# Optimization experiments

Measured on AMD Instinct MI355X. Metric: run time of the kernel, lower is better.

The kernel has to match this reference:

```python
import jax, jax.numpy as jnp
import numpy as np

MAX_TOKENS = 8192
MAX_NUM_NODES = 8192
FEATURES = 256


def setup_inputs() -> dict:
    key = jax.random.key(0)
    k_emb, k_start, k_end = jax.random.split(key, 3)
    embedding = jax.random.normal(k_emb, (MAX_NUM_NODES, FEATURES), dtype=jnp.float32)
    node_span_starts = jax.random.randint(k_start, (MAX_NUM_NODES,), 0, 4096, dtype=jnp.int32)
    node_span_ends = jax.random.randint(k_end, (MAX_NUM_NODES,), 0, MAX_TOKENS, dtype=jnp.int32)
    return {
        "embedding": embedding,
        "node_span_starts": node_span_starts,
        "node_span_ends": node_span_ends,
        "num_nodes": 6000,
    }


def reference(embedding, node_span_starts, node_span_ends, num_nodes):
    # For each token t: out[t] = sum over valid nodes n with start_n <= t <= end_n of embedding[n].
    # Identical math to the original vmap+where+sum, expressed as a masked matmul
    # to avoid the O(N*T*F) dense intermediate.
    t = jnp.arange(MAX_TOKENS)[:, None]                      # [T, 1]
    node_valid = jnp.arange(MAX_NUM_NODES) < num_nodes       # [N]
    in_span = (node_span_starts[None, :] <= t) & (t <= node_span_ends[None, :])  # [T, N]
    mask = (in_span & node_valid[None, :]).astype(embedding.dtype)               # [T, N]
    return mask @ embedding                                  # [T, F]
```

## Files before the change

kernel.cpp:

```cpp
#include <hip/hip_runtime.h>

#define T_TOKENS 8192
#define MAX_NODES 8192
#define FEAT 256
#define NCHUNKS 256
#define CHUNK 32
#define MAX_EV 512

__device__ __forceinline__ void classify_events(
    const int* __restrict__ starts, const int* __restrict__ ends,
    int num_nodes, int row_lo, int row_hi, int tid,
    int* s_list, int* s_cnt) {
    const int4* starts4 = (const int4*)starts;
    const int4* ends4 = (const int4*)ends;
#pragma unroll
    for (int r = 0; r < MAX_NODES / 1024; ++r) {
        const int vec = r * 256 + tid;
        const int4 s4 = starts4[vec];
        const int4 e4 = ends4[vec];
        const int sv[4] = {s4.x, s4.y, s4.z, s4.w};
        const int ev[4] = {e4.x, e4.y, e4.z, e4.w};
        const int nbase = vec * 4;
#pragma unroll
        for (int k = 0; k < 4; ++k) {
            const int node = nbase + k;
            const int s = sv[k];
            const int e = ev[k];
            if (node < num_nodes && s <= e && s < T_TOKENS && e >= 0) {
                const int sc = s < 0 ? 0 : s;
                if (sc >= row_lo && sc < row_hi) {
                    int p = atomicAdd(s_cnt, 1);
                    if (p < MAX_EV) s_list[p] = (node << 6) | ((sc - row_lo) << 1);
                }
                const int e1 = e + 1;
                if (e1 < T_TOKENS && e1 >= row_lo && e1 < row_hi) {
                    int p = atomicAdd(s_cnt, 1);
                    if (p < MAX_EV) s_list[p] = (node << 6) | ((e1 - row_lo) << 1) | 1;
                }
            }
        }
    }
}

__global__ __launch_bounds__(FEAT) void colsum_kernel(
    const float* __restrict__ emb,
    const int* __restrict__ starts,
    const int* __restrict__ ends,
    const int* __restrict__ num_nodes_p,
    float* __restrict__ colsum) {
    __shared__ int s_list[MAX_EV];
    __shared__ int s_cnt;
    const int c = blockIdx.x;
    const int f = threadIdx.x;
    const int num_nodes = *num_nodes_p;
    const int row_lo = c * CHUNK;
    const int row_hi = row_lo + CHUNK;

    if (f == 0) s_cnt = 0;
    __syncthreads();
    classify_events(starts, ends, num_nodes, row_lo, row_hi, f, s_list, &s_cnt);
    __syncthreads();
    const int cnt = min(s_cnt, MAX_EV);

    float acc = 0.f;
    int j = 0;
    for (; j + 4 <= cnt; j += 4) {
        const int e0 = s_list[j + 0], e1 = s_list[j + 1];
        const int e2 = s_list[j + 2], e3 = s_list[j + 3];
        const float v0 = emb[(size_t)(e0 >> 6) * FEAT + f];
        const float v1 = emb[(size_t)(e1 >> 6) * FEAT + f];
        const float v2 = emb[(size_t)(e2 >> 6) * FEAT + f];
        const float v3 = emb[(size_t)(e3 >> 6) * FEAT + f];
        acc += (e0 & 1) ? -v0 : v0;
        acc += (e1 & 1) ? -v1 : v1;
        acc += (e2 & 1) ? -v2 : v2;
        acc += (e3 & 1) ? -v3 : v3;
    }
    for (; j < cnt; ++j) {
        const int e0 = s_list[j];
        const float v0 = emb[(size_t)(e0 >> 6) * FEAT + f];
        acc += (e0 & 1) ? -v0 : v0;
    }
    colsum[(size_t)c * FEAT + f] = acc;
}

__global__ __launch_bounds__(FEAT) void scan_kernel(
    const float* __restrict__ emb,
    const int* __restrict__ starts,
    const int* __restrict__ ends,
    const int* __restrict__ num_nodes_p,
    const float* __restrict__ colsum,
    float* __restrict__ out) {
    __shared__ int s_list[MAX_EV];
    __shared__ int s_cnt;
    __shared__ float s_diff[CHUNK * FEAT];
    const int c = blockIdx.x;
    const int f = threadIdx.x;
    const int num_nodes = *num_nodes_p;
    const int row_lo = c * CHUNK;
    const int row_hi = row_lo + CHUNK;

#pragma unroll
    for (int r = 0; r < CHUNK; ++r) s_diff[r * FEAT + f] = 0.f;

    if (f == 0) s_cnt = 0;
    __syncthreads();
    classify_events(starts, ends, num_nodes, row_lo, row_hi, f, s_list, &s_cnt);
    __syncthreads();
    const int cnt = min(s_cnt, MAX_EV);

    float a0 = 0.f, a1 = 0.f, a2 = 0.f, a3 = 0.f;
    float a4 = 0.f, a5 = 0.f, a6 = 0.f, a7 = 0.f;
    int i = 0;
    for (; i + 8 <= c; i += 8) {
        a0 += colsum[(size_t)(i + 0) * FEAT + f];
        a1 += colsum[(size_t)(i + 1) * FEAT + f];
        a2 += colsum[(size_t)(i + 2) * FEAT + f];
        a3 += colsum[(size_t)(i + 3) * FEAT + f];
        a4 += colsum[(size_t)(i + 4) * FEAT + f];
        a5 += colsum[(size_t)(i + 5) * FEAT + f];
        a6 += colsum[(size_t)(i + 6) * FEAT + f];
        a7 += colsum[(size_t)(i + 7) * FEAT + f];
    }
    for (; i < c; ++i) a0 += colsum[(size_t)i * FEAT + f];
    float run = ((a0 + a1) + (a2 + a3)) + ((a4 + a5) + (a6 + a7));

    int j = 0;
    for (; j + 4 <= cnt; j += 4) {
        const int e0 = s_list[j + 0], e1 = s_list[j + 1];
        const int e2 = s_list[j + 2], e3 = s_list[j + 3];
        const float v0 = emb[(size_t)(e0 >> 6) * FEAT + f];
        const float v1 = emb[(size_t)(e1 >> 6) * FEAT + f];
        const float v2 = emb[(size_t)(e2 >> 6) * FEAT + f];
        const float v3 = emb[(size_t)(e3 >> 6) * FEAT + f];
        s_diff[((e0 >> 1) & 31) * FEAT + f] += (e0 & 1) ? -v0 : v0;
        s_diff[((e1 >> 1) & 31) * FEAT + f] += (e1 & 1) ? -v1 : v1;
        s_diff[((e2 >> 1) & 31) * FEAT + f] += (e2 & 1) ? -v2 : v2;
        s_diff[((e3 >> 1) & 31) * FEAT + f] += (e3 & 1) ? -v3 : v3;
    }
    for (; j < cnt; ++j) {
        const int e0 = s_list[j];
        const float v0 = emb[(size_t)(e0 >> 6) * FEAT + f];
        s_diff[((e0 >> 1) & 31) * FEAT + f] += (e0 & 1) ? -v0 : v0;
    }

    float* o = out + (size_t)row_lo * FEAT + f;
#pragma unroll
    for (int r = 0; r < CHUNK; ++r) {
        run += s_diff[r * FEAT + f];
        o[r * FEAT] = run;
    }
}

extern "C" void kernel_launch(void* const* d_in, const int* in_sizes, int n_in,
                              void* d_out, int out_size, void* d_ws, size_t ws_size,
                              hipStream_t stream) {
    const float* emb     = (const float*)d_in[0];
    const int* starts    = (const int*)d_in[1];
    const int* ends      = (const int*)d_in[2];
    const int* num_nodes = (const int*)d_in[3];
    float* out           = (float*)d_out;

    float* colsum = (float*)d_ws;

    colsum_kernel<<<NCHUNKS, FEAT, 0, stream>>>(emb, starts, ends, num_nodes,
                                                colsum);
    scan_kernel<<<NCHUNKS, FEAT, 0, stream>>>(emb, starts, ends, num_nodes,
                                              colsum, out);
}
```

Measured before the change: 90.83 us.

## Fuse colsum and scan kernels into one cooperative kernel with grid sync

Merges the two-kernel design into a single cooperative launch. Each block classifies the span events and scatters them into its shared diff buffer once, derives its chunk column sum from that buffer, writes it out, then waits on a grid-wide sync before the prefix over earlier chunks and the final scan. This removes the duplicate event classification and gather from the first kernel, along with one launch boundary. In exchange it adds a cooperative launch and a grid barrier, which requires all 256 blocks to be co-resident.

```diff
diff --git a/kernel.cpp b/kernel.cpp
--- a/kernel.cpp
+++ b/kernel.cpp
@@ -1,4 +1,7 @@
 #include <hip/hip_runtime.h>
+#include <hip/hip_cooperative_groups.h>
+
+namespace cg = cooperative_groups;
 
 #define T_TOKENS 8192
 #define MAX_NODES 8192
@@ -7,93 +10,17 @@
 #define CHUNK 32
 #define MAX_EV 512
 
-__device__ __forceinline__ void classify_events(
-    const int* __restrict__ starts, const int* __restrict__ ends,
-    int num_nodes, int row_lo, int row_hi, int tid,
-    int* s_list, int* s_cnt) {
-    const int4* starts4 = (const int4*)starts;
-    const int4* ends4 = (const int4*)ends;
-#pragma unroll
-    for (int r = 0; r < MAX_NODES / 1024; ++r) {
-        const int vec = r * 256 + tid;
-        const int4 s4 = starts4[vec];
-        const int4 e4 = ends4[vec];
-        const int sv[4] = {s4.x, s4.y, s4.z, s4.w};
-        const int ev[4] = {e4.x, e4.y, e4.z, e4.w};
-        const int nbase = vec * 4;
-#pragma unroll
-        for (int k = 0; k < 4; ++k) {
-            const int node = nbase + k;
-            const int s = sv[k];
-            const int e = ev[k];
-            if (node < num_nodes && s <= e && s < T_TOKENS && e >= 0) {
-                const int sc = s < 0 ? 0 : s;
-                if (sc >= row_lo && sc < row_hi) {
-                    int p = atomicAdd(s_cnt, 1);
-                    if (p < MAX_EV) s_list[p] = (node << 6) | ((sc - row_lo) << 1);
-                }
-                const int e1 = e + 1;
-                if (e1 < T_TOKENS && e1 >= row_lo && e1 < row_hi) {
-                    int p = atomicAdd(s_cnt, 1);
-                    if (p < MAX_EV) s_list[p] = (node << 6) | ((e1 - row_lo) << 1) | 1;
-                }
-            }
-        }
-    }
-}
-
-__global__ __launch_bounds__(FEAT) void colsum_kernel(
+__global__ __launch_bounds__(FEAT) void fused_span_kernel(
     const float* __restrict__ emb,
     const int* __restrict__ starts,
     const int* __restrict__ ends,
     const int* __restrict__ num_nodes_p,
-    float* __restrict__ colsum) {
+    float* __restrict__ colsum,
+    float* __restrict__ out) {
+    __shared__ float s_diff[CHUNK * FEAT];
     __shared__ int s_list[MAX_EV];
     __shared__ int s_cnt;
-    const int c = blockIdx.x;
-    const int f = threadIdx.x;
-    const int num_nodes = *num_nodes_p;
-    const int row_lo = c * CHUNK;
-    const int row_hi = row_lo + CHUNK;
 
-    if (f == 0) s_cnt = 0;
-    __syncthreads();
-    classify_events(starts, ends, num_nodes, row_lo, row_hi, f, s_list, &s_cnt);
-    __syncthreads();
-    const int cnt = min(s_cnt, MAX_EV);
-
-    float acc = 0.f;
-    int j = 0;
-    for (; j + 4 <= cnt; j += 4) {
-        const int e0 = s_list[j + 0], e1 = s_list[j + 1];
-        const int e2 = s_list[j + 2], e3 = s_list[j + 3];
-        const float v0 = emb[(size_t)(e0 >> 6) * FEAT + f];
-        const float v1 = emb[(size_t)(e1 >> 6) * FEAT + f];
-        const float v2 = emb[(size_t)(e2 >> 6) * FEAT + f];
-        const float v3 = emb[(size_t)(e3 >> 6) * FEAT + f];
-        acc += (e0 & 1) ? -v0 : v0;
-        acc += (e1 & 1) ? -v1 : v1;
-        acc += (e2 & 1) ? -v2 : v2;
-        acc += (e3 & 1) ? -v3 : v3;
-    }
-    for (; j < cnt; ++j) {
-        const int e0 = s_list[j];
-        const float v0 = emb[(size_t)(e0 >> 6) * FEAT + f];
-        acc += (e0 & 1) ? -v0 : v0;
-    }
-    colsum[(size_t)c * FEAT + f] = acc;
-}
-
-__global__ __launch_bounds__(FEAT) void scan_kernel(
-    const float* __restrict__ emb,
-    const int* __restrict__ starts,
-    const int* __restrict__ ends,
-    const int* __restrict__ num_nodes_p,
-    const float* __restrict__ colsum,
-    float* __restrict__ out) {
-    __shared__ int s_list[MAX_EV];
-    __shared__ int s_cnt;
-    __shared__ float s_diff[CHUNK * FEAT];
     const int c = blockIdx.x;
     const int f = threadIdx.x;
     const int num_nodes = *num_nodes_p;
@@ -102,28 +29,44 @@
 
 #pragma unroll
     for (int r = 0; r < CHUNK; ++r) s_diff[r * FEAT + f] = 0.f;
-
     if (f == 0) s_cnt = 0;
     __syncthreads();
-    classify_events(starts, ends, num_nodes, row_lo, row_hi, f, s_list, &s_cnt);
+
+    {
+        const int4* starts4 = (const int4*)starts;
+        const int4* ends4 = (const int4*)ends;
+#pragma unroll
+        for (int r = 0; r < MAX_NODES / 1024; ++r) {
+            const int vec = r * 256 + f;
+            const int4 s4 = starts4[vec];
+            const int4 e4 = ends4[vec];
+            const int sv[4] = {s4.x, s4.y, s4.z, s4.w};
+            const int evv[4] = {e4.x, e4.y, e4.z, e4.w};
+            const int nbase = vec * 4;
+#pragma unroll
+            for (int k = 0; k < 4; ++k) {
+                const int node = nbase + k;
+                const int s = sv[k];
+                const int e = evv[k];
+                if (node < num_nodes && s <= e && s < T_TOKENS && e >= 0) {
+                    const int sc = s < 0 ? 0 : s;
+                    if (sc >= row_lo && sc < row_hi) {
+                        int p = atomicAdd(&s_cnt, 1);
+                        if (p < MAX_EV)
+                            s_list[p] = (node << 6) | ((sc - row_lo) << 1);
+                    }
+                    const int e1 = e + 1;
+                    if (e1 < T_TOKENS && e1 >= row_lo && e1 < row_hi) {
+                        int p = atomicAdd(&s_cnt, 1);
+                        if (p < MAX_EV)
+                            s_list[p] = (node << 6) | ((e1 - row_lo) << 1) | 1;
+                    }
+                }
+            }
+        }
+    }
     __syncthreads();
     const int cnt = min(s_cnt, MAX_EV);
-
-    float a0 = 0.f, a1 = 0.f, a2 = 0.f, a3 = 0.f;
-    float a4 = 0.f, a5 = 0.f, a6 = 0.f, a7 = 0.f;
-    int i = 0;
-    for (; i + 8 <= c; i += 8) {
-        a0 += colsum[(size_t)(i + 0) * FEAT + f];
-        a1 += colsum[(size_t)(i + 1) * FEAT + f];
-        a2 += colsum[(size_t)(i + 2) * FEAT + f];
-        a3 += colsum[(size_t)(i + 3) * FEAT + f];
-        a4 += colsum[(size_t)(i + 4) * FEAT + f];
-        a5 += colsum[(size_t)(i + 5) * FEAT + f];
-        a6 += colsum[(size_t)(i + 6) * FEAT + f];
-        a7 += colsum[(size_t)(i + 7) * FEAT + f];
-    }
-    for (; i < c; ++i) a0 += colsum[(size_t)i * FEAT + f];
-    float run = ((a0 + a1) + (a2 + a3)) + ((a4 + a5) + (a6 + a7));
 
     int j = 0;
     for (; j + 4 <= cnt; j += 4) {
@@ -144,6 +87,29 @@
         s_diff[((e0 >> 1) & 31) * FEAT + f] += (e0 & 1) ? -v0 : v0;
     }
 
+    float acc = 0.f;
+#pragma unroll
+    for (int r = 0; r < CHUNK; ++r) acc += s_diff[r * FEAT + f];
+    colsum[(size_t)c * FEAT + f] = acc;
+
+    cg::this_grid().sync();
+
+    float a0 = 0.f, a1 = 0.f, a2 = 0.f, a3 = 0.f;
+    float a4 = 0.f, a5 = 0.f, a6 = 0.f, a7 = 0.f;
+    int i = 0;
+    for (; i + 8 <= c; i += 8) {
+        a0 += colsum[(size_t)(i + 0) * FEAT + f];
+        a1 += colsum[(size_t)(i + 1) * FEAT + f];
+        a2 += colsum[(size_t)(i + 2) * FEAT + f];
+        a3 += colsum[(size_t)(i + 3) * FEAT + f];
+        a4 += colsum[(size_t)(i + 4) * FEAT + f];
+        a5 += colsum[(size_t)(i + 5) * FEAT + f];
+        a6 += colsum[(size_t)(i + 6) * FEAT + f];
+        a7 += colsum[(size_t)(i + 7) * FEAT + f];
+    }
+    for (; i < c; ++i) a0 += colsum[(size_t)i * FEAT + f];
+    float run = ((a0 + a1) + (a2 + a3)) + ((a4 + a5) + (a6 + a7));
+
     float* o = out + (size_t)row_lo * FEAT + f;
 #pragma unroll
     for (int r = 0; r < CHUNK; ++r) {
@@ -160,11 +126,10 @@
     const int* ends      = (const int*)d_in[2];
     const int* num_nodes = (const int*)d_in[3];
     float* out           = (float*)d_out;
+    float* colsum        = (float*)d_ws;
 
-    float* colsum = (float*)d_ws;
-
-    colsum_kernel<<<NCHUNKS, FEAT, 0, stream>>>(emb, starts, ends, num_nodes,
-                                                colsum);
-    scan_kernel<<<NCHUNKS, FEAT, 0, stream>>>(emb, starts, ends, num_nodes,
-                                              colsum, out);
+    void* args[] = {(void*)&emb, (void*)&starts, (void*)&ends,
+                    (void*)&num_nodes, (void*)&colsum, (void*)&out};
+    hipLaunchCooperativeKernel((void*)fused_span_kernel, dim3(NCHUNKS),
+                               dim3(FEAT), args, 0, stream);
 }
```

New measurement: 135.4 us. 1.49x slower.

## Split event lists across 4 warp slices and add separate prefix-sum kernel

Applied to the files above, without the earlier changes.

Blocks grow to 1024 threads, split into four slices that process interleaved events. Colsum partials are reduced in shared memory, and the scan kernel uses shared atomics on the diff buffer plus a per-slice sub-prefix. A new single-block prefix kernel computes chunk prefixes, so the scan kernel no longer sums all preceding colsums per block (quadratic reads). This adds one launch and shared-memory atomics in exchange.

```diff
diff --git a/kernel.cpp b/kernel.cpp
--- a/kernel.cpp
+++ b/kernel.cpp
@@ -5,7 +5,10 @@
 #define FEAT 256
 #define NCHUNKS 256
 #define CHUNK 32
-#define MAX_EV 512
+#define NSLICE 4
+#define BLOCK (NSLICE * FEAT)
+#define MAX_EV 1024
+#define ROWS_PER_SLICE (CHUNK / NSLICE)
 
 __device__ __forceinline__ void classify_events(
     const int* __restrict__ starts, const int* __restrict__ ends,
@@ -14,8 +17,8 @@
     const int4* starts4 = (const int4*)starts;
     const int4* ends4 = (const int4*)ends;
 #pragma unroll
-    for (int r = 0; r < MAX_NODES / 1024; ++r) {
-        const int vec = r * 256 + tid;
+    for (int r = 0; r < 2; ++r) {
+        const int vec = tid * 2 + r;
         const int4 s4 = starts4[vec];
         const int4 e4 = ends4[vec];
         const int sv[4] = {s4.x, s4.y, s4.z, s4.w};
@@ -42,7 +45,7 @@
     }
 }
 
-__global__ __launch_bounds__(FEAT) void colsum_kernel(
+__global__ __launch_bounds__(BLOCK) void colsum_kernel(
     const float* __restrict__ emb,
     const int* __restrict__ starts,
     const int* __restrict__ ends,
@@ -50,23 +53,28 @@
     float* __restrict__ colsum) {
     __shared__ int s_list[MAX_EV];
     __shared__ int s_cnt;
+    __shared__ float s_part[NSLICE][FEAT];
+    const int tid = threadIdx.x;
+    const int f = tid & (FEAT - 1);
+    const int g = tid >> 8;
     const int c = blockIdx.x;
-    const int f = threadIdx.x;
     const int num_nodes = *num_nodes_p;
     const int row_lo = c * CHUNK;
     const int row_hi = row_lo + CHUNK;
 
-    if (f == 0) s_cnt = 0;
-    __syncthreads();
-    classify_events(starts, ends, num_nodes, row_lo, row_hi, f, s_list, &s_cnt);
+    if (tid == 0) s_cnt = 0;
+    __syncthreads();
+    classify_events(starts, ends, num_nodes, row_lo, row_hi, tid, s_list, &s_cnt);
     __syncthreads();
     const int cnt = min(s_cnt, MAX_EV);
 
     float acc = 0.f;
-    int j = 0;
-    for (; j + 4 <= cnt; j += 4) {
-        const int e0 = s_list[j + 0], e1 = s_list[j + 1];
-        const int e2 = s_list[j + 2], e3 = s_list[j + 3];
+    int j = g;
+    for (; j + 3 * NSLICE < cnt; j += 4 * NSLICE) {
+        const int e0 = s_list[j];
+        const int e1 = s_list[j + NSLICE];
+        const int e2 = s_list[j + 2 * NSLICE];
+        const int e3 = s_list[j + 3 * NSLICE];
         const float v0 = emb[(size_t)(e0 >> 6) * FEAT + f];
         const float v1 = emb[(size_t)(e1 >> 6) * FEAT + f];
         const float v2 = emb[(size_t)(e2 >> 6) * FEAT + f];
@@ -76,78 +84,110 @@
         acc += (e2 & 1) ? -v2 : v2;
         acc += (e3 & 1) ? -v3 : v3;
     }
-    for (; j < cnt; ++j) {
+    for (; j < cnt; j += NSLICE) {
         const int e0 = s_list[j];
         const float v0 = emb[(size_t)(e0 >> 6) * FEAT + f];
         acc += (e0 & 1) ? -v0 : v0;
     }
-    colsum[(size_t)c * FEAT + f] = acc;
-}
-
-__global__ __launch_bounds__(FEAT) void scan_kernel(
+    s_part[g][f] = acc;
+    __syncthreads();
+    if (g == 0)
+        colsum[(size_t)c * FEAT + f] =
+            (s_part[0][f] + s_part[1][f]) + (s_part[2][f] + s_part[3][f]);
+}
+
+__global__ __launch_bounds__(BLOCK) void prefix_kernel(
+    const float* __restrict__ colsum,
+    float* __restrict__ pfx) {
+    __shared__ float s_tot[NSLICE][FEAT];
+    const int tid = threadIdx.x;
+    const int f = tid & (FEAT - 1);
+    const int g = tid >> 8;
+    const int base_row = g * (NCHUNKS / NSLICE);
+
+    float vals[NCHUNKS / NSLICE];
+    float tot = 0.f;
+#pragma unroll
+    for (int i = 0; i < NCHUNKS / NSLICE; ++i) {
+        vals[i] = colsum[(size_t)(base_row + i) * FEAT + f];
+        tot += vals[i];
+    }
+    s_tot[g][f] = tot;
+    __syncthreads();
+    float run = 0.f;
+    for (int gg = 0; gg < g; ++gg) run += s_tot[gg][f];
+#pragma unroll
+    for (int i = 0; i < NCHUNKS / NSLICE; ++i) {
+        pfx[(size_t)(base_row + i) * FEAT + f] = run;
+        run += vals[i];
+    }
+}
+
+__global__ __launch_bounds__(BLOCK) void scan_kernel(
     const float* __restrict__ emb,
     const int* __restrict__ starts,
     const int* __restrict__ ends,
     const int* __restrict__ num_nodes_p,
-    const float* __restrict__ colsum,
+    const float* __restrict__ pfx,
     float* __restrict__ out) {
+    __shared__ float s_diff[CHUNK * FEAT];
     __shared__ int s_list[MAX_EV];
     __shared__ int s_cnt;
-    __shared__ float s_diff[CHUNK * FEAT];
+    __shared__ float s_sub[NSLICE][FEAT];
+    const int tid = threadIdx.x;
+    const int f = tid & (FEAT - 1);
+    const int g = tid >> 8;
     const int c = blockIdx.x;
-    const int f = threadIdx.x;
     const int num_nodes = *num_nodes_p;
     const int row_lo = c * CHUNK;
     const int row_hi = row_lo + CHUNK;
 
 #pragma unroll
-    for (int r = 0; r < CHUNK; ++r) s_diff[r * FEAT + f] = 0.f;
-
-    if (f == 0) s_cnt = 0;
-    __syncthreads();
-    classify_events(starts, ends, num_nodes, row_lo, row_hi, f, s_list, &s_cnt);
+    for (int r = 0; r < ROWS_PER_SLICE; ++r)
+        s_diff[(g * ROWS_PER_SLICE + r) * FEAT + f] = 0.f;
+    if (tid == 0) s_cnt = 0;
+    __syncthreads();
+
+    classify_events(starts, ends, num_nodes, row_lo, row_hi, tid, s_list, &s_cnt);
     __syncthreads();
     const int cnt = min(s_cnt, MAX_EV);
 
-    float a0 = 0.f, a1 = 0.f, a2 = 0.f, a3 = 0.f;
-    float a4 = 0.f, a5 = 0.f, a6 = 0.f, a7 = 0.f;
-    int i = 0;
-    for (; i + 8 <= c; i += 8) {
-        a0 += colsum[(size_t)(i + 0) * FEAT + f];
-        a1 += colsum[(size_t)(i + 1) * FEAT + f];
-        a2 += colsum[(size_t)(i + 2) * FEAT + f];
-        a3 += colsum[(size_t)(i + 3) * FEAT + f];
-        a4 += colsum[(size_t)(i + 4) * FEAT + f];
-        a5 += colsum[(size_t)(i + 5) * FEAT + f];
-        a6 += colsum[(size_t)(i + 6) * FEAT + f];
-        a7 += colsum[(size_t)(i + 7) * FEAT + f];
-    }
-    for (; i < c; ++i) a0 += colsum[(size_t)i * FEAT + f];
-    float run = ((a0 + a1) + (a2 + a3)) + ((a4 + a5) + (a6 + a7));
-
-    int j = 0;
-    for (; j + 4 <= cnt; j += 4) {
-        const int e0 = s_list[j + 0], e1 = s_list[j + 1];
-        const int e2 = s_list[j + 2], e3 = s_list[j + 3];
+    int j = g;
+    for (; j + 3 * NSLICE < cnt; j += 4 * NSLICE) {
+        const int e0 = s_list[j];
+        const int e1 = s_list[j + NSLICE];
+        const int e2 = s_list[j + 2 * NSLICE];
+        const int e3 = s_list[j + 3 * NSLICE];
         const float v0 = emb[(size_t)(e0 >> 6) * FEAT + f];
         const float v1 = emb[(size_t)(e1 >> 6) * FEAT + f];
         const float v2 = emb[(size_t)(e2 >> 6) * FEAT + f];
         const float v3 = emb[(size_t)(e3 >> 6) * FEAT + f];
-        s_diff[((e0 >> 1) & 31) * FEAT + f] += (e0 & 1) ? -v0 : v0;
-        s_diff[((e1 >> 1) & 31) * FEAT + f] += (e1 & 1) ? -v1 : v1;
-        s_diff[((e2 >> 1) & 31) * FEAT + f] += (e2 & 1) ? -v2 : v2;
-        s_diff[((e3 >> 1) & 31) * FEAT + f] += (e3 & 1) ? -v3 : v3;
-    }
-    for (; j < cnt; ++j) {
-        const int e0 = s_list[j];
-        const float v0 = emb[(size_t)(e0 >> 6) * FEAT + f];
-        s_diff[((e0 >> 1) & 31) * FEAT + f] += (e0 & 1) ? -v0 : v0;
-    }
-
-    float* o = out + (size_t)row_lo * FEAT + f;
-#pragma unroll
-    for (int r = 0; r < CHUNK; ++r) {
-        run += s_diff[r * FEAT + f];
+        atomicAdd(&s_diff[((e0 >> 1) & 31) * FEAT + f], (e0 & 1) ? -v0 : v0);
+        atomicAdd(&s_diff[((e1 >> 1) & 31) * FEAT + f], (e1 & 1) ? -v1 : v1);
+        atomicAdd(&s_diff[((e2 >> 1) & 31) * FEAT + f], (e2 & 1) ? -v2 : v2);
+        atomicAdd(&s_diff[((e3 >> 1) & 31) * FEAT + f], (e3 & 1) ? -v3 : v3);
+    }
+    for (; j < cnt; j += NSLICE) {
+        const int e0 = s_list[j];
+        const float v0 = emb[(size_t)(e0 >> 6) * FEAT + f];
+        atomicAdd(&s_diff[((e0 >> 1) & 31) * FEAT + f], (e0 & 1) ? -v0 : v0);
+    }
+    __syncthreads();
+
+    float sub = 0.f;
+#pragma unroll
+    for (int r = 0; r < ROWS_PER_SLICE; ++r)
+        sub += s_diff[(g * ROWS_PER_SLICE + r) * FEAT + f];
+    s_sub[g][f] = sub;
+    __syncthreads();
+
+    float run = pfx[(size_t)c * FEAT + f];
+    for (int gg = 0; gg < g; ++gg) run += s_sub[gg][f];
+
+    float* o = out + (size_t)(row_lo + g * ROWS_PER_SLICE) * FEAT + f;
+#pragma unroll
+    for (int r = 0; r < ROWS_PER_SLICE; ++r) {
+        run += s_diff[(g * ROWS_PER_SLICE + r) * FEAT + f];
         o[r * FEAT] = run;
     }
 }
@@ -162,9 +202,11 @@
     float* out           = (float*)d_out;
 
     float* colsum = (float*)d_ws;
-
-    colsum_kernel<<<NCHUNKS, FEAT, 0, stream>>>(emb, starts, ends, num_nodes,
-                                                colsum);
-    scan_kernel<<<NCHUNKS, FEAT, 0, stream>>>(emb, starts, ends, num_nodes,
-                                              colsum, out);
-}
+    float* pfx    = colsum + (size_t)NCHUNKS * FEAT;
+
+    colsum_kernel<<<NCHUNKS, BLOCK, 0, stream>>>(emb, starts, ends, num_nodes,
+                                                 colsum);
+    prefix_kernel<<<1, BLOCK, 0, stream>>>(colsum, pfx);
+    scan_kernel<<<NCHUNKS, BLOCK, 0, stream>>>(emb, starts, ends, num_nodes,
+                                               pfx, out);
+}
```

Measured after the change: 119.7 us. 31.8% more time.
